# Kernel tuning notes

Measured on AMD Instinct MI355X. Metric: run time of the kernel, lower is better.

Reference implementation:

```python
import jax, jax.numpy as jnp
import numpy as np
from math import sqrt

D_MODEL = 1024
HEADS = 16
D_K = D_MODEL // HEADS
NEG = -1e9


def setup_inputs() -> dict:
    key = jax.random.key(0)
    ks = jax.random.split(key, 8)
    bs, s, d = 2, 2048, D_MODEL
    inp = {
        "k": jax.random.normal(ks[0], (bs, s, d), jnp.float32),
        "v": jax.random.normal(ks[1], (bs, s, d), jnp.float32),
        "q": jax.random.normal(ks[2], (bs, s, d), jnp.float32),
        "mask": jax.random.randint(ks[3], (bs, s, 1), 0, 2).astype(jnp.int64),
        # torch nn.Linear weights: y = x @ W.T, W is [out, in]
        "Wq": jax.random.normal(ks[4], (d, d), jnp.float32) / sqrt(d),
        "Wk": jax.random.normal(ks[5], (d, d), jnp.float32) / sqrt(d),
        "Wv": jax.random.normal(ks[6], (d, d), jnp.float32) / sqrt(d),
        "Wo": jax.random.normal(ks[7], (d, d), jnp.float32) / sqrt(d),
    }
    return inp


def reference(k, v, q, mask, Wq, Wk, Wv, Wo):
    bs, s_k, d = k.shape
    s_q = q.shape[1]
    h, d_k = HEADS, D_K
    # linear projections (no bias), then split heads -> [bs, h, s, d_k]
    kh = (k @ Wk.T).reshape(bs, s_k, h, d_k).transpose(0, 2, 1, 3)
    vh = (v @ Wv.T).reshape(bs, s_k, h, d_k).transpose(0, 2, 1, 3)
    qh = (q @ Wq.T).reshape(bs, s_q, h, d_k).transpose(0, 2, 1, 3)
    # scaled dot-product scores [bs, h, s_q, s_k]
    scores = jnp.einsum("bhqd,bhkd->bhqk", qh, kh) / sqrt(d_k)
    # mask [bs, s_k, 1] -> [bs, 1, 1, s_k], masked positions get -1e9
    m = mask[:, None].transpose(0, 1, 3, 2)  # [bs,1,1,s_k]
    scores = jnp.where(m == 0, NEG, scores)
    probs = jax.nn.softmax(scores, axis=-1)  # dropout is identity (eval)
    attn = jnp.einsum("bhqk,bhkd->bhqd", probs, vh)
    attn_concat = attn.transpose(0, 2, 1, 3).reshape(bs, s_q, d)
    return attn_concat @ Wo.T
```

## Files before the change

### kernel.cpp

```cpp
#include <hip/hip_runtime.h>

typedef __bf16 bf16x8 __attribute__((ext_vector_type(8)));
typedef float f32x4 __attribute__((ext_vector_type(4)));

#define BS 2
#define SEQ 2048
#define DM 1024
#define NH 16
#define DKH 64
#define GM 4096
#define GN 1024
#define GK 1024
#define NEGV (-1e9f)

#define OFF_XQ 0u
#define OFF_XK 4194304u
#define OFF_XV 8388608u
#define OFF_WQ 12582912u
#define OFF_WK 13631488u
#define OFF_WV 14680064u
#define OFF_WO 15728640u
#define OFF_QH 16777216u
#define OFF_KH 20971520u
#define OFF_VH 25165824u
#define OFF_KC OFF_XQ
#define OFF_VT OFF_XK
#define OFF_AT OFF_VH

#if __has_builtin(__builtin_amdgcn_exp2f)
#define EXP2(x) __builtin_amdgcn_exp2f(x)
#else
static __device__ __forceinline__ float EXP2(float x) {
    float r;
    asm volatile("v_exp_f32 %0, %1" : "=v"(r) : "v"(x));
    return r;
}
#endif

__device__ __forceinline__ unsigned cvt_pk(float lo, float hi) {
    unsigned r;
    asm volatile("v_cvt_pk_bf16_f32 %0, %1, %2" : "=v"(r) : "v"(lo), "v"(hi));
    return r;
}

__device__ __forceinline__ unsigned short f2b(float f) {
    unsigned u = __builtin_bit_cast(unsigned, f);
    u += 0x7fffu + ((u >> 16) & 1u);
    return (unsigned short)(u >> 16);
}

typedef const __attribute__((address_space(1))) unsigned int* gas_t;
typedef __attribute__((address_space(3))) unsigned int* las_t;

__device__ __forceinline__ void gload_lds16(const ushort* g, ushort* l) {
    __builtin_amdgcn_global_load_lds((gas_t)(const void*)g, (las_t)(void*)l, 16, 0, 0);
}

__global__ __launch_bounds__(256)
void cvt_kernel(const float* __restrict__ q, const float* __restrict__ k,
                const float* __restrict__ v, const float* __restrict__ wq,
                const float* __restrict__ wk, const float* __restrict__ wv,
                const float* __restrict__ wo, ushort* __restrict__ ws)
{
    const float* src; unsigned n; unsigned dst;
    switch (blockIdx.y) {
        case 0: src = q;  n = 4194304u; dst = OFF_XQ; break;
        case 1: src = k;  n = 4194304u; dst = OFF_XK; break;
        case 2: src = v;  n = 4194304u; dst = OFF_XV; break;
        case 3: src = wq; n = 1048576u; dst = OFF_WQ; break;
        case 4: src = wk; n = 1048576u; dst = OFF_WK; break;
        case 5: src = wv; n = 1048576u; dst = OFF_WV; break;
        default: src = wo; n = 1048576u; dst = OFF_WO; break;
    }
    unsigned i = (blockIdx.x * 256u + threadIdx.x) * 4u;
    if (i >= n) return;
    float4 f = *(const float4*)(src + i);
    ushort4 o;
    o.x = f2b(f.x); o.y = f2b(f.y); o.z = f2b(f.z); o.w = f2b(f.w);
    *(ushort4*)(ws + dst + i) = o;
}

template<bool PROJ>
__global__ __launch_bounds__(256)
void gemm_bt(const ushort* __restrict__ Abase, const ushort* __restrict__ Bbase,
             ushort* __restrict__ obf, float* __restrict__ of)
{
    __shared__ __align__(16) ushort lA[128 * 64];
    __shared__ __align__(16) ushort lB[128 * 64];

    const ushort* A = Abase;
    const ushort* Bw = Bbase;
    ushort* dst = obf;
    float scale = 1.0f;
    if (PROJ) {
        unsigned z = blockIdx.z;
        A  += (size_t)z * (GM * GK);
        Bw += (size_t)z * (GN * GK);
        dst += (size_t)z * (GM * GN);
        if (z == 0) scale = 0.125f * 1.44269504088896f;
    }

    const int tid = threadIdx.x;
    const int lane = tid & 63, wid = tid >> 6;
    const int wr = wid >> 1, wc = wid & 1;
    const int lr = lane & 15, lg = lane >> 4;
    const int m0 = blockIdx.y * 128, n0 = blockIdx.x * 128;
    const int srow = wid * 32 + (lane >> 3);
    const int scol = (lane & 7) * 8;

    f32x4 acc[4][4] = {};

    for (int k0 = 0; k0 < GK; k0 += 64) {
        __syncthreads();
#pragma unroll
        for (int p = 0; p < 4; ++p) {
            gload_lds16(A + (size_t)(m0 + srow + p * 8) * GK + k0 + scol,
                        &lA[(wid * 32 + p * 8) * 64]);
            gload_lds16(Bw + (size_t)(n0 + srow + p * 8) * GK + k0 + scol,
                        &lB[(wid * 32 + p * 8) * 64]);
        }
        __syncthreads();
#pragma unroll
        for (int kk = 0; kk < 2; ++kk) {
            bf16x8 af[4], bfr[4];
#pragma unroll
            for (int i = 0; i < 4; ++i) {
                af[i]  = *(const bf16x8*)(&lA[(wr * 64 + i * 16 + lr) * 64 + kk * 32 + lg * 8]);
                bfr[i] = *(const bf16x8*)(&lB[(wc * 64 + i * 16 + lr) * 64 + kk * 32 + lg * 8]);
            }
#pragma unroll
            for (int i = 0; i < 4; ++i)
#pragma unroll
                for (int j = 0; j < 4; ++j)
                    acc[i][j] = __builtin_amdgcn_mfma_f32_16x16x32_bf16(af[i], bfr[j], acc[i][j], 0, 0, 0);
        }
    }

#pragma unroll
    for (int i = 0; i < 4; ++i) {
#pragma unroll
        for (int j = 0; j < 4; ++j) {
            int col = n0 + wc * 64 + j * 16 + lr;
#pragma unroll
            for (int r = 0; r < 4; ++r) {
                int row = m0 + wr * 64 + i * 16 + lg * 4 + r;
                float val = acc[i][j][r] * scale;
                if (PROJ) {
                    int b = row >> 11, s = row & 2047;
                    int hh = col >> 6, dk = col & 63;
                    dst[(((size_t)b * NH + hh) * SEQ + s) * DKH + dk] = f2b(val);
                } else {
                    of[(size_t)row * GN + col] = val;
                }
            }
        }
    }
}

__global__ __launch_bounds__(256)
void scan_kernel(const int* __restrict__ mask, int* __restrict__ idx, int* __restrict__ mbuf)
{
    const int b = blockIdx.x;
    const int* mp = mask + (size_t)b * SEQ;
    const int tid = threadIdx.x;
    const int lane = tid & 63, w = tid >> 6;
    int v[8];
    int cnt = 0;
#pragma unroll
    for (int j = 0; j < 8; ++j) { v[j] = mp[tid * 8 + j]; cnt += (v[j] != 0); }
    int inc = cnt;
#pragma unroll
    for (int d = 1; d < 64; d <<= 1) {
        int t = __shfl_up(inc, d);
        if (lane >= d) inc += t;
    }
    __shared__ int wsum[4];
    if (lane == 63) wsum[w] = inc;
    __syncthreads();
    int base = inc - cnt;
    for (int i = 0; i < w; ++i) base += wsum[i];
    int c = base;
    int* ob = idx + (size_t)b * SEQ;
#pragma unroll
    for (int j = 0; j < 8; ++j)
        if (v[j] != 0) ob[c++] = tid * 8 + j;
    if (tid == 255) mbuf[b] = base + cnt;
}

__global__ __launch_bounds__(256)
void gather_kernel(ushort* __restrict__ ws, const int* __restrict__ idx,
                   const int* __restrict__ mbuf)
{
    const int t = blockIdx.x;
    const int bh = blockIdx.y;
    const int b = bh >> 4;
    const int mb = mbuf[b];
    if (t * 64 >= mb) return;
    const int* ix = idx + (size_t)b * SEQ;
    const ushort* Kh = ws + OFF_KH + (size_t)bh * (SEQ * DKH);
    const ushort* Vh = ws + OFF_VH + (size_t)bh * (SEQ * DKH);
    ushort* Kc = ws + OFF_KC + (size_t)bh * (SEQ * DKH);
    ushort* VT = ws + OFF_VT + (size_t)bh * (DKH * SEQ);

    __shared__ __align__(16) ushort lv[64][72];
    const int tid = threadIdx.x;

#pragma unroll
    for (int it = 0; it < 2; ++it) {
        int g = it * 256 + tid;
        int row = g >> 3, gi = g & 7;
        int ck = t * 64 + row;
        uint4 kv = {0, 0, 0, 0}, vv = {0, 0, 0, 0};
        if (ck < mb) kv = *(const uint4*)(Kh + (size_t)ix[ck] * DKH + gi * 8);
        *(uint4*)(Kc + (size_t)ck * DKH + gi * 8) = kv;
        int cv = t * 64 + ((row & 3) * 16 + (row >> 2));
        if (cv < mb) vv = *(const uint4*)(Vh + (size_t)ix[cv] * DKH + gi * 8);
        *(uint4*)(&lv[row][gi * 8]) = vv;
    }
    __syncthreads();
#pragma unroll
    for (int it = 0; it < 2; ++it) {
        int g = it * 256 + tid;
        int d = g >> 3, gp = g & 7;
        ushort tmp[8];
#pragma unroll
        for (int j = 0; j < 8; ++j) tmp[j] = lv[gp * 8 + j][d];
        *(uint4*)(VT + (size_t)d * SEQ + t * 64 + gp * 8) = *(const uint4*)tmp;
    }
}

__global__ __launch_bounds__(256)
void attn_kernel(ushort* __restrict__ ws, const int* __restrict__ mbuf)
{
    const int bid = blockIdx.x;
    const int qt = bid & 31;
    const int h  = (bid >> 5) & 15;
    const int b  = bid >> 9;
    const int bh = b * NH + h;

    const ushort* Qp = ws + OFF_QH + (size_t)bh * (SEQ * DKH);
    const ushort* Kc = ws + OFF_KC + (size_t)bh * (SEQ * DKH);
    const ushort* VT = ws + OFF_VT + (size_t)bh * (DKH * SEQ);
    ushort* At = ws + OFF_AT;

    const int mb = mbuf[b];
    const int nt = (mb + 63) >> 6;

    __shared__ __align__(16) ushort lK[2][64 * 64];
    __shared__ __align__(16) ushort lV[2][64 * 64];
    __shared__ __align__(16) ushort lP[4][16][72];

    const int tid = threadIdx.x;
    const int lane = tid & 63, wid = tid >> 6;
    const int lr = lane & 15, lg = lane >> 4;
    ushort* lPw = &lP[wid][0][0];

    const int srow = wid * 16 + (lane >> 3);
    const int sg = lane & 7;

    const int qrow0 = qt * 64 + wid * 16;
    bf16x8 qf[2];
#pragma unroll
    for (int kk = 0; kk < 2; ++kk)
        qf[kk] = *(const bf16x8*)(Qp + (size_t)(qrow0 + lr) * DKH + kk * 32 + lg * 8);

    f32x4 acc_o[4] = {};
    float lrun[4] = {0.f, 0.f, 0.f, 0.f};

    auto STAGE = [&](int buf, int kt) {
        const int kbase = kt * 64;
#pragma unroll
        for (int c = 0; c < 2; ++c) {
            int r = srow + c * 8;
            gload_lds16(Kc + (size_t)(kbase + r) * DKH + ((sg ^ (r & 7)) * 8),
                        &lK[buf][(wid * 16 + c * 8) * 64]);
            gload_lds16(VT + (size_t)r * SEQ + kbase + ((sg ^ (r & 7)) * 8),
                        &lV[buf][(wid * 16 + c * 8) * 64]);
        }
    };

    STAGE(0, 0);
    __syncthreads();

    for (int kt = 0; kt < nt; ++kt) {
        const int cur = kt & 1;
        if (kt + 1 < nt) STAGE(cur ^ 1, kt + 1);
        const ushort* lKc = lK[cur];
        const ushort* lVc = lV[cur];

        f32x4 s[4];
#pragma unroll
        for (int fc = 0; fc < 4; ++fc) {
            int row = fc * 16 + lr;
            int sw = row & 7;
            bf16x8 kf0 = *(const bf16x8*)(lKc + row * 64 + ((lg ^ sw) * 8));
            bf16x8 kf1 = *(const bf16x8*)(lKc + row * 64 + (((4 + lg) ^ sw) * 8));
            f32x4 t = {};
            t = __builtin_amdgcn_mfma_f32_16x16x32_bf16(qf[0], kf0, t, 0, 0, 0);
            t = __builtin_amdgcn_mfma_f32_16x16x32_bf16(qf[1], kf1, t, 0, 0, 0);
            s[fc] = t;
        }

        if (kt == nt - 1) {
            const int kbase = kt * 64;
#pragma unroll
            for (int fc = 0; fc < 4; ++fc)
                if (kbase + fc * 16 + lr >= mb)
                    s[fc] = f32x4{NEGV, NEGV, NEGV, NEGV};
        }

#pragma unroll
        for (int r = 0; r < 4; ++r) {
            float p0 = EXP2(s[0][r]), p1 = EXP2(s[1][r]);
            float p2 = EXP2(s[2][r]), p3 = EXP2(s[3][r]);
            lrun[r] += (p0 + p1) + (p2 + p3);
            uint2 pk;
            pk.x = cvt_pk(p0, p1);
            pk.y = cvt_pk(p2, p3);
            *(uint2*)(lPw + (lg * 4 + r) * 72 + lr * 4) = pk;
        }

#pragma unroll
        for (int kk = 0; kk < 2; ++kk) {
            bf16x8 pf = *(const bf16x8*)(lPw + lr * 72 + kk * 32 + lg * 8);
#pragma unroll
            for (int fc2 = 0; fc2 < 4; ++fc2) {
                int d = fc2 * 16 + lr;
                bf16x8 vf = *(const bf16x8*)(lVc + d * 64 + (((kk * 4 + lg) ^ (d & 7)) * 8));
                acc_o[fc2] = __builtin_amdgcn_mfma_f32_16x16x32_bf16(pf, vf, acc_o[fc2], 0, 0, 0);
            }
        }
        __syncthreads();
    }

#pragma unroll
    for (int r = 0; r < 4; ++r) {
        float l = lrun[r];
        l += __shfl_xor(l, 1);
        l += __shfl_xor(l, 2);
        l += __shfl_xor(l, 4);
        l += __shfl_xor(l, 8);
        float rl = 1.0f / l;
        int qrow = qrow0 + lg * 4 + r;
#pragma unroll
        for (int fc2 = 0; fc2 < 4; ++fc2)
            At[((size_t)(b * SEQ) + qrow) * DM + h * DKH + fc2 * 16 + lr] =
                f2b(acc_o[fc2][r] * rl);
    }
}

extern "C" void kernel_launch(void* const* d_in, const int* in_sizes, int n_in,
                              void* d_out, int out_size, void* d_ws, size_t ws_size,
                              hipStream_t stream) {
    const float* kin = (const float*)d_in[0];
    const float* vin = (const float*)d_in[1];
    const float* qin = (const float*)d_in[2];
    const int*   msk = (const int*)d_in[3];
    const float* wq  = (const float*)d_in[4];
    const float* wk  = (const float*)d_in[5];
    const float* wv  = (const float*)d_in[6];
    const float* wo  = (const float*)d_in[7];
    ushort* ws = (ushort*)d_ws;
    float* out = (float*)d_out;
    int* idxb = (int*)(ws + OFF_WQ);
    int* mbuf = idxb + 4096;

    cvt_kernel<<<dim3(4096, 7), 256, 0, stream>>>(qin, kin, vin, wq, wk, wv, wo, ws);
    gemm_bt<true><<<dim3(8, 32, 3), 256, 0, stream>>>(ws + OFF_XQ, ws + OFF_WQ, ws + OFF_QH, nullptr);
    scan_kernel<<<2, 256, 0, stream>>>(msk, idxb, mbuf);
    gather_kernel<<<dim3(32, 32), 256, 0, stream>>>(ws, idxb, mbuf);
    attn_kernel<<<1024, 256, 0, stream>>>(ws, mbuf);
    gemm_bt<false><<<dim3(8, 32, 1), 256, 0, stream>>>(ws + OFF_AT, ws + OFF_WO, nullptr, out);
}
```

Baseline: 140.1 us.

## Fuse mask compaction scatter into projection GEMM epilogue, drop gather kernel

The mask scan now emits a per-position compacted index, and the K/V projection GEMM epilogue scatters directly into compacted K and pre-swizzled transposed V layouts, eliminating the separate gather/transpose kernel and its extra round-trip through memory. The GEMM also gets a block-index swizzle for better tile locality, and the attention kernel raises wave priority around MFMA sections. The scan scratch is placed in the output buffer before the final GEMM overwrites it; V^T writes are strided scalar stores which may be less coalesced.

```diff
diff --git a/kernel.cpp b/kernel.cpp
--- a/kernel.cpp
+++ b/kernel.cpp
@@ -21,11 +21,9 @@
 #define OFF_WV 14680064u
 #define OFF_WO 15728640u
 #define OFF_QH 16777216u
-#define OFF_KH 20971520u
-#define OFF_VH 25165824u
-#define OFF_KC OFF_XQ
-#define OFF_VT OFF_XK
-#define OFF_AT OFF_VH
+#define OFF_KC 20971520u
+#define OFF_VT 25165824u
+#define OFF_AT OFF_XQ
 
 #if __has_builtin(__builtin_amdgcn_exp2f)
 #define EXP2(x) __builtin_amdgcn_exp2f(x)
@@ -80,85 +78,8 @@
     *(ushort4*)(ws + dst + i) = o;
 }
 
-template<bool PROJ>
 __global__ __launch_bounds__(256)
-void gemm_bt(const ushort* __restrict__ Abase, const ushort* __restrict__ Bbase,
-             ushort* __restrict__ obf, float* __restrict__ of)
-{
-    __shared__ __align__(16) ushort lA[128 * 64];
-    __shared__ __align__(16) ushort lB[128 * 64];
-
-    const ushort* A = Abase;
-    const ushort* Bw = Bbase;
-    ushort* dst = obf;
-    float scale = 1.0f;
-    if (PROJ) {
-        unsigned z = blockIdx.z;
-        A  += (size_t)z * (GM * GK);
-        Bw += (size_t)z * (GN * GK);
-        dst += (size_t)z * (GM * GN);
-        if (z == 0) scale = 0.125f * 1.44269504088896f;
-    }
-
-    const int tid = threadIdx.x;
-    const int lane = tid & 63, wid = tid >> 6;
-    const int wr = wid >> 1, wc = wid & 1;
-    const int lr = lane & 15, lg = lane >> 4;
-    const int m0 = blockIdx.y * 128, n0 = blockIdx.x * 128;
-    const int srow = wid * 32 + (lane >> 3);
-    const int scol = (lane & 7) * 8;
-
-    f32x4 acc[4][4] = {};
-
-    for (int k0 = 0; k0 < GK; k0 += 64) {
-        __syncthreads();
-#pragma unroll
-        for (int p = 0; p < 4; ++p) {
-            gload_lds16(A + (size_t)(m0 + srow + p * 8) * GK + k0 + scol,
-                        &lA[(wid * 32 + p * 8) * 64]);
-            gload_lds16(Bw + (size_t)(n0 + srow + p * 8) * GK + k0 + scol,
-                        &lB[(wid * 32 + p * 8) * 64]);
-        }
-        __syncthreads();
-#pragma unroll
-        for (int kk = 0; kk < 2; ++kk) {
-            bf16x8 af[4], bfr[4];
-#pragma unroll
-            for (int i = 0; i < 4; ++i) {
-                af[i]  = *(const bf16x8*)(&lA[(wr * 64 + i * 16 + lr) * 64 + kk * 32 + lg * 8]);
-                bfr[i] = *(const bf16x8*)(&lB[(wc * 64 + i * 16 + lr) * 64 + kk * 32 + lg * 8]);
-            }
-#pragma unroll
-            for (int i = 0; i < 4; ++i)
-#pragma unroll
-                for (int j = 0; j < 4; ++j)
-                    acc[i][j] = __builtin_amdgcn_mfma_f32_16x16x32_bf16(af[i], bfr[j], acc[i][j], 0, 0, 0);
-        }
-    }
-
-#pragma unroll
-    for (int i = 0; i < 4; ++i) {
-#pragma unroll
-        for (int j = 0; j < 4; ++j) {
-            int col = n0 + wc * 64 + j * 16 + lr;
-#pragma unroll
-            for (int r = 0; r < 4; ++r) {
-                int row = m0 + wr * 64 + i * 16 + lg * 4 + r;
-                float val = acc[i][j][r] * scale;
-                if (PROJ) {
-                    int b = row >> 11, s = row & 2047;
-                    int hh = col >> 6, dk = col & 63;
-                    dst[(((size_t)b * NH + hh) * SEQ + s) * DKH + dk] = f2b(val);
-                } else {
-                    of[(size_t)row * GN + col] = val;
-                }
-            }
-        }
-    }
-}
-
-__global__ __launch_bounds__(256)
-void scan_kernel(const int* __restrict__ mask, int* __restrict__ idx, int* __restrict__ mbuf)
+void scan_kernel(const int* __restrict__ mask, int* __restrict__ cpos, int* __restrict__ mbuf)
 {
     const int b = blockIdx.x;
     const int* mp = mask + (size_t)b * SEQ;
@@ -180,52 +101,125 @@
     int base = inc - cnt;
     for (int i = 0; i < w; ++i) base += wsum[i];
     int c = base;
-    int* ob = idx + (size_t)b * SEQ;
-#pragma unroll
-    for (int j = 0; j < 8; ++j)
-        if (v[j] != 0) ob[c++] = tid * 8 + j;
+    int* ob = cpos + (size_t)b * SEQ;
+#pragma unroll
+    for (int j = 0; j < 8; ++j) {
+        ob[tid * 8 + j] = (v[j] != 0) ? c : -1;
+        c += (v[j] != 0);
+    }
     if (tid == 255) mbuf[b] = base + cnt;
 }
 
+template<bool PROJ>
 __global__ __launch_bounds__(256)
-void gather_kernel(ushort* __restrict__ ws, const int* __restrict__ idx,
-                   const int* __restrict__ mbuf)
+void gemm_bt(const ushort* __restrict__ Abase, const ushort* __restrict__ Bbase,
+             ushort* __restrict__ wsbase, float* __restrict__ of,
+             const int* __restrict__ cpos)
 {
-    const int t = blockIdx.x;
-    const int bh = blockIdx.y;
-    const int b = bh >> 4;
-    const int mb = mbuf[b];
-    if (t * 64 >= mb) return;
-    const int* ix = idx + (size_t)b * SEQ;
-    const ushort* Kh = ws + OFF_KH + (size_t)bh * (SEQ * DKH);
-    const ushort* Vh = ws + OFF_VH + (size_t)bh * (SEQ * DKH);
-    ushort* Kc = ws + OFF_KC + (size_t)bh * (SEQ * DKH);
-    ushort* VT = ws + OFF_VT + (size_t)bh * (DKH * SEQ);
-
-    __shared__ __align__(16) ushort lv[64][72];
+    __shared__ __align__(16) ushort lA[128 * 64];
+    __shared__ __align__(16) ushort lB[128 * 64];
+
+    const ushort* A = Abase;
+    const ushort* Bw = Bbase;
+    float scale = 1.0f;
+    if (PROJ) {
+        unsigned z = blockIdx.z;
+        A  += (size_t)z * (GM * GK);
+        Bw += (size_t)z * (GN * GK);
+        if (z == 0) scale = 0.125f * 1.44269504088896f;
+    }
+
     const int tid = threadIdx.x;
-
-#pragma unroll
-    for (int it = 0; it < 2; ++it) {
-        int g = it * 256 + tid;
-        int row = g >> 3, gi = g & 7;
-        int ck = t * 64 + row;
-        uint4 kv = {0, 0, 0, 0}, vv = {0, 0, 0, 0};
-        if (ck < mb) kv = *(const uint4*)(Kh + (size_t)ix[ck] * DKH + gi * 8);
-        *(uint4*)(Kc + (size_t)ck * DKH + gi * 8) = kv;
-        int cv = t * 64 + ((row & 3) * 16 + (row >> 2));
-        if (cv < mb) vv = *(const uint4*)(Vh + (size_t)ix[cv] * DKH + gi * 8);
-        *(uint4*)(&lv[row][gi * 8]) = vv;
-    }
-    __syncthreads();
-#pragma unroll
-    for (int it = 0; it < 2; ++it) {
-        int g = it * 256 + tid;
-        int d = g >> 3, gp = g & 7;
-        ushort tmp[8];
-#pragma unroll
-        for (int j = 0; j < 8; ++j) tmp[j] = lv[gp * 8 + j][d];
-        *(uint4*)(VT + (size_t)d * SEQ + t * 64 + gp * 8) = *(const uint4*)tmp;
+    const int lane = tid & 63, wid = tid >> 6;
+    const int wr = wid >> 1, wc = wid & 1;
+    const int lr = lane & 15, lg = lane >> 4;
+    const int lin = blockIdx.y * 8 + blockIdx.x;
+    const int swz = (lin & 7) * 32 + (lin >> 3);
+    const int m0 = (swz >> 3) * 128, n0 = (swz & 7) * 128;
+    const int srow = wid * 32 + (lane >> 3);
+    const int scol = (lane & 7) * 8;
+
+    f32x4 acc[4][4] = {};
+
+    for (int k0 = 0; k0 < GK; k0 += 64) {
+        __syncthreads();
+#pragma unroll
+        for (int p = 0; p < 4; ++p) {
+            gload_lds16(A + (size_t)(m0 + srow + p * 8) * GK + k0 + scol,
+                        &lA[(wid * 32 + p * 8) * 64]);
+            gload_lds16(Bw + (size_t)(n0 + srow + p * 8) * GK + k0 + scol,
+                        &lB[(wid * 32 + p * 8) * 64]);
+        }
+        __syncthreads();
+#pragma unroll
+        for (int kk = 0; kk < 2; ++kk) {
+            bf16x8 af[4], bfr[4];
+#pragma unroll
+            for (int i = 0; i < 4; ++i) {
+                af[i]  = *(const bf16x8*)(&lA[(wr * 64 + i * 16 + lr) * 64 + kk * 32 + lg * 8]);
+                bfr[i] = *(const bf16x8*)(&lB[(wc * 64 + i * 16 + lr) * 64 + kk * 32 + lg * 8]);
+            }
+#pragma unroll
+            for (int i = 0; i < 4; ++i)
+#pragma unroll
+                for (int j = 0; j < 4; ++j)
+                    acc[i][j] = __builtin_amdgcn_mfma_f32_16x16x32_bf16(af[i], bfr[j], acc[i][j], 0, 0, 0);
+        }
+    }
+
+    if (PROJ) {
+        const int z = blockIdx.z;
+        ushort* qh = wsbase + OFF_QH;
+        ushort* kc = wsbase + OFF_KC;
+        ushort* vtp = wsbase + OFF_VT;
+#pragma unroll
+        for (int i = 0; i < 4; ++i) {
+#pragma unroll
+            for (int r = 0; r < 4; ++r) {
+                int row = m0 + wr * 64 + i * 16 + lg * 4 + r;
+                int b = row >> 11, s = row & 2047;
+                if (z == 0) {
+#pragma unroll
+                    for (int j = 0; j < 4; ++j) {
+                        int col = n0 + wc * 64 + j * 16 + lr;
+                        qh[(((size_t)b * NH + (col >> 6)) * SEQ + s) * DKH + (col & 63)] =
+                            f2b(acc[i][j][r] * scale);
+                    }
+                } else {
+                    int c = cpos[b * SEQ + s];
+                    if (c >= 0) {
+                        if (z == 1) {
+#pragma unroll
+                            for (int j = 0; j < 4; ++j) {
+                                int col = n0 + wc * 64 + j * 16 + lr;
+                                kc[(((size_t)b * NH + (col >> 6)) * SEQ + c) * DKH + (col & 63)] =
+                                    f2b(acc[i][j][r]);
+                            }
+                        } else {
+                            int vt = (c & ~63) | ((c & 15) * 4 + ((c >> 4) & 3));
+#pragma unroll
+                            for (int j = 0; j < 4; ++j) {
+                                int col = n0 + wc * 64 + j * 16 + lr;
+                                vtp[(((size_t)b * NH + (col >> 6)) * DKH + (col & 63)) * SEQ + vt] =
+                                    f2b(acc[i][j][r]);
+                            }
+                        }
+                    }
+                }
+            }
+        }
+    } else {
+#pragma unroll
+        for (int i = 0; i < 4; ++i)
+#pragma unroll
+            for (int j = 0; j < 4; ++j) {
+                int col = n0 + wc * 64 + j * 16 + lr;
+#pragma unroll
+                for (int r = 0; r < 4; ++r) {
+                    int row = m0 + wr * 64 + i * 16 + lg * 4 + r;
+                    of[(size_t)row * GN + col] = acc[i][j][r];
+                }
+            }
     }
 }
 
@@ -289,6 +283,7 @@
         const ushort* lVc = lV[cur];
 
         f32x4 s[4];
+        __builtin_amdgcn_s_setprio(1);
 #pragma unroll
         for (int fc = 0; fc < 4; ++fc) {
             int row = fc * 16 + lr;
@@ -300,6 +295,7 @@
             t = __builtin_amdgcn_mfma_f32_16x16x32_bf16(qf[1], kf1, t, 0, 0, 0);
             s[fc] = t;
         }
+        __builtin_amdgcn_s_setprio(0);
 
         if (kt == nt - 1) {
             const int kbase = kt * 64;
@@ -320,6 +316,7 @@
             *(uint2*)(lPw + (lg * 4 + r) * 72 + lr * 4) = pk;
         }
 
+        __builtin_amdgcn_s_setprio(1);
 #pragma unroll
         for (int kk = 0; kk < 2; ++kk) {
             bf16x8 pf = *(const bf16x8*)(lPw + lr * 72 + kk * 32 + lg * 8);
@@ -330,6 +327,7 @@
                 acc_o[fc2] = __builtin_amdgcn_mfma_f32_16x16x32_bf16(pf, vf, acc_o[fc2], 0, 0, 0);
             }
         }
+        __builtin_amdgcn_s_setprio(0);
         __syncthreads();
     }
 
@@ -362,13 +360,12 @@
     const float* wo  = (const float*)d_in[7];
     ushort* ws = (ushort*)d_ws;
     float* out = (float*)d_out;
-    int* idxb = (int*)(ws + OFF_WQ);
-    int* mbuf = idxb + 4096;
-
+    int* cposb = (int*)d_out;
+    int* mbuf = cposb + BS * SEQ;
+
+    scan_kernel<<<2, 256, 0, stream>>>(msk, cposb, mbuf);
     cvt_kernel<<<dim3(4096, 7), 256, 0, stream>>>(qin, kin, vin, wq, wk, wv, wo, ws);
-    gemm_bt<true><<<dim3(8, 32, 3), 256, 0, stream>>>(ws + OFF_XQ, ws + OFF_WQ, ws + OFF_QH, nullptr);
-    scan_kernel<<<2, 256, 0, stream>>>(msk, idxb, mbuf);
-    gather_kernel<<<dim3(32, 32), 256, 0, stream>>>(ws, idxb, mbuf);
+    gemm_bt<true><<<dim3(8, 32, 3), 256, 0, stream>>>(ws + OFF_XQ, ws + OFF_WQ, ws, nullptr, cposb);
     attn_kernel<<<1024, 256, 0, stream>>>(ws, mbuf);
-    gemm_bt<false><<<dim3(8, 32, 1), 256, 0, stream>>>(ws + OFF_AT, ws + OFF_WO, nullptr, out);
-}
+    gemm_bt<false><<<dim3(8, 32, 1), 256, 0, stream>>>(ws + OFF_AT, ws + OFF_WO, ws, out, nullptr);
+}
```

New measurement: 141.1 us. No clear change (+0.7%).
